# Kernel optimization log

Measured on AMD Instinct MI355X. Metric: run time of the kernel, lower is better.

## Reference

```python
import jax, jax.numpy as jnp
import numpy as np

B, T, D = 32, 4096, 96        # batch, frames, codebook_dim
N_CB, K = 6, 384              # n_codebooks, codebook_size
PROJ, W2V = 192, 768          # semantic_proj_dim, w2v_bert_dim
COMMIT = 0.5


def setup_inputs() -> dict:
    key = jax.random.key(0)
    ks = jax.random.split(key, 7)
    z = jax.random.normal(ks[0], (B, T, D), jnp.float32)
    w2v_targets = jax.random.normal(ks[1], (B, T, W2V), jnp.float32)
    # torch init: uniform(-1/K, 1/K) per codebook
    codebooks = jax.random.uniform(ks[2], (N_CB, K, D), jnp.float32, -1.0 / K, 1.0 / K)
    w1 = jax.random.normal(ks[3], (D, PROJ), jnp.float32) * 0.02
    b1 = jnp.zeros((PROJ,), jnp.float32)
    w2 = jax.random.normal(ks[4], (PROJ, W2V), jnp.float32) * 0.02
    b2 = jnp.zeros((W2V,), jnp.float32)
    return {"z": z, "w2v_targets": w2v_targets, "codebooks": codebooks,
            "w1": w1, "b1": b1, "w2": w2, "b2": b2}


def _quantize(residual, emb):
    """One VQ stage: squared-L2 nearest code + gather. residual: (B,T,D), emb: (K,D)."""
    flat = residual.reshape(-1, D)                                   # (BT, D)
    dist = (jnp.sum(flat * flat, axis=1, keepdims=True)
            - 2.0 * flat @ emb.T
            + jnp.sum(emb * emb, axis=1))                            # (BT, K)
    idx = jnp.argmin(dist, axis=1).reshape(B, T)                     # (B, T)
    z_q = emb[idx]                                                   # (B, T, D) gather
    return z_q, idx


def reference(z, w2v_targets, codebooks, w1, b1, w2, b2):
    sg = jax.lax.stop_gradient
    residual = z
    z_q_total = jnp.zeros_like(z)
    codes = []
    vq_loss = jnp.float32(0.0)
    semantic_loss = jnp.float32(0.0)
    for i in range(N_CB):
        z_q, idx = _quantize(residual, codebooks[i])
        commitment_loss = jnp.mean((sg(z_q) - residual) ** 2)
        embedding_loss = jnp.mean((z_q - sg(residual)) ** 2)
        vq_loss = vq_loss + embedding_loss + COMMIT * commitment_loss
        z_q_st = residual + sg(z_q - residual)                       # straight-through
        if i == 0:
            h = jax.nn.gelu(z_q_st @ w1 + b1, approximate=False)
            pred = h @ w2 + b2                                       # (B, T, W2V)
            semantic_loss = jnp.mean((pred - w2v_targets) ** 2)
        z_q_total = z_q_total + z_q_st
        residual = residual - sg(z_q_st)
        codes.append(idx)
    all_codes = jnp.stack(codes, axis=-1)                            # (B, T, N_CB)
    return z_q_total, all_codes, vq_loss, semantic_loss
```

## Files before the change

kernel.cpp:

```cpp
#include <hip/hip_runtime.h>
#include <hip/hip_bf16.h>

#define BT    131072
#define DD    96
#define KCB   384
#define NCB   6
#define PROJ  192
#define W2V   768

#define ZQT_OFF   0L
#define CODES_OFF 12582912L
#define VQ_OFF    13369344L
#define SEM_OFF   13369345L

#define ACC_OFF   0L
#define E32_OFF   64L
#define W1T_OFF   9280L
#define W2T_OFF   46144L

#define TT 4
#define CT 24
#define TB 256

typedef __attribute__((ext_vector_type(8))) short  bf16x8;
typedef __attribute__((ext_vector_type(4))) float  f32x4;

static __device__ __forceinline__ unsigned short f2bf(float x) {
    __hip_bfloat16 h = __float2bfloat16(x);
    return *reinterpret_cast<unsigned short*>(&h);
}
static __device__ __forceinline__ float comp(const float4& v, int c) {
    return c == 0 ? v.x : c == 1 ? v.y : c == 2 ? v.z : v.w;
}

static __device__ __forceinline__ float pairwise96_sq(const float4* r) {
    float a[8];
#pragma unroll
    for (int j = 0; j < 8; ++j) {
        const int c = j & 3, base = j >> 2;
        float x0 = comp(r[base], c);
        float s  = __fmul_rn(x0, x0);
#pragma unroll
        for (int t = 1; t < 12; ++t) {
            float x = comp(r[base + 2 * t], c);
            s = __fadd_rn(s, __fmul_rn(x, x));
        }
        a[j] = s;
    }
    return __fadd_rn(__fadd_rn(__fadd_rn(a[0], a[1]), __fadd_rn(a[2], a[3])),
                     __fadd_rn(__fadd_rn(a[4], a[5]), __fadd_rn(a[6], a[7])));
}

__global__ void kzero(double* __restrict__ acc) {
    if (threadIdx.x < 8) acc[threadIdx.x] = 0.0;
}

__global__ void kee(const float* __restrict__ cb, float* __restrict__ E32) {
    int c = blockIdx.x * 256 + threadIdx.x;
    if (c < NCB * KCB) {
        const float* row = cb + (size_t)c * DD;
        float a[8];
#pragma unroll
        for (int j = 0; j < 8; ++j) a[j] = __fmul_rn(row[j], row[j]);
        for (int t = 1; t < 12; ++t) {
#pragma unroll
            for (int j = 0; j < 8; ++j) {
                float x = row[8 * t + j];
                a[j] = __fadd_rn(a[j], __fmul_rn(x, x));
            }
        }
        E32[c] = __fadd_rn(__fadd_rn(__fadd_rn(a[0], a[1]), __fadd_rn(a[2], a[3])),
                           __fadd_rn(__fadd_rn(a[4], a[5]), __fadd_rn(a[6], a[7])));
    }
}

__global__ void kwt(const float* __restrict__ w1, const float* __restrict__ w2,
                    __hip_bfloat16* __restrict__ w1T, __hip_bfloat16* __restrict__ w2T) {
    int i = blockIdx.x * 256 + threadIdx.x;
    if (i < DD * PROJ) {
        int n = i / DD, k = i % DD;
        w1T[i] = __float2bfloat16(w1[k * PROJ + n]);
    }
    int j = i - DD * PROJ;
    if (j >= 0 && j < PROJ * W2V) {
        int n = j / PROJ, k = j % PROJ;
        w2T[j] = __float2bfloat16(w2[k * W2V + n]);
    }
}

__global__ __launch_bounds__(256, 2) void kq2(
        const float* __restrict__ z, const float* __restrict__ cb,
        const float* __restrict__ E32, float* __restrict__ dout,
        float4* __restrict__ rg) {
    __shared__ __align__(16) float  e_lds[4][CT * DD];
    __shared__ __align__(16) float2 comb[4][TB];
    __shared__ __align__(16) float  S_lds[TB];

    const int tid = threadIdx.x, lane = tid & 63, w = tid >> 6;
    const long tok0 = (long)blockIdx.x * TB;

    {
        const long t = tok0 + tid;
        const float4* z4 = (const float4*)(z + t * DD);
        float4 r[24];
#pragma unroll
        for (int i = 0; i < 24; ++i) r[i] = z4[i];
        S_lds[tid] = pairwise96_sq(r);
#pragma unroll
        for (int i = 0; i < 24; ++i) rg[(long)i * BT + t] = r[i];
    }
    __syncthreads();

#pragma unroll 1
    for (int s = 0; s < NCB; ++s) {
        float Sj[TT];
#pragma unroll
        for (int j = 0; j < TT; ++j) Sj[j] = S_lds[64 * j + lane];
        float mv[TT]; int bi[TT];
#pragma unroll
        for (int j = 0; j < TT; ++j) { mv[j] = 3.4e38f; bi[j] = 0; }

#pragma unroll 1
        for (int ct = 0; ct < 96 / CT; ++ct) {
            const int cbase = w * 96 + ct * CT;
            {
                const float4* esrc = (const float4*)(cb + ((size_t)s * KCB + cbase) * DD);
                float4* edst = (float4*)&e_lds[w][0];
#pragma unroll
                for (int i = 0; i < 9; ++i) edst[i * 64 + lane] = esrc[i * 64 + lane];
            }
            float acc[CT][TT];
#pragma unroll
            for (int c = 0; c < CT; ++c)
#pragma unroll
                for (int j = 0; j < TT; ++j) acc[c][j] = 0.f;

            float4 rv[TT];
#pragma unroll
            for (int j = 0; j < TT; ++j) rv[j] = rg[tok0 + 64 * j + lane];
#pragma unroll 1
            for (int kt = 0; kt < 24; ++kt) {
                float4 rnx[TT];
                if (kt < 23) {
#pragma unroll
                    for (int j = 0; j < TT; ++j)
                        rnx[j] = rg[(long)(kt + 1) * BT + tok0 + 64 * j + lane];
                }
                float4 r2[TT];
#pragma unroll
                for (int j = 0; j < TT; ++j) {
                    r2[j].x = __fmul_rn(2.f, rv[j].x); r2[j].y = __fmul_rn(2.f, rv[j].y);
                    r2[j].z = __fmul_rn(2.f, rv[j].z); r2[j].w = __fmul_rn(2.f, rv[j].w);
                }
                const float* eb = &e_lds[w][kt * 4];
#pragma unroll
                for (int c = 0; c < CT; ++c) {
                    float4 e = *(const float4*)(eb + c * DD);
#pragma unroll
                    for (int j = 0; j < TT; ++j) {
                        acc[c][j] = fmaf(r2[j].x, e.x, acc[c][j]);
                        acc[c][j] = fmaf(r2[j].y, e.y, acc[c][j]);
                        acc[c][j] = fmaf(r2[j].z, e.z, acc[c][j]);
                        acc[c][j] = fmaf(r2[j].w, e.w, acc[c][j]);
                    }
                }
#pragma unroll
                for (int j = 0; j < TT; ++j) rv[j] = rnx[j];
            }
#pragma unroll
            for (int c = 0; c < CT; ++c) {
                const float E = E32[s * KCB + cbase + c];
#pragma unroll
                for (int j = 0; j < TT; ++j) {
                    float d = __fadd_rn(__fsub_rn(Sj[j], acc[c][j]), E);
                    if (d < mv[j]) { mv[j] = d; bi[j] = cbase + c; }
                }
            }
        }
#pragma unroll
        for (int j = 0; j < TT; ++j)
            comb[w][64 * j + lane] = make_float2(mv[j], (float)bi[j]);
        __syncthreads();

        {
            const long t = tok0 + tid;
            float bv = comb[0][tid].x; int bidx = (int)comb[0][tid].y;
#pragma unroll
            for (int w2 = 1; w2 < 4; ++w2) {
                float2 cnd = comb[w2][tid];
                if (cnd.x < bv) { bv = cnd.x; bidx = (int)cnd.y; }
            }
            dout[CODES_OFF + t * NCB + s] = (float)bidx;
            if (s < NCB - 1) {
                const float4* q4 = (const float4*)(cb + ((size_t)s * KCB + bidx) * DD);
                float4 rn[24];
#pragma unroll
                for (int i = 0; i < 24; ++i) {
                    float4 rv = rg[(long)i * BT + t], q = q4[i];
                    float4 d, st;
                    d.x = __fsub_rn(q.x, rv.x); d.y = __fsub_rn(q.y, rv.y);
                    d.z = __fsub_rn(q.z, rv.z); d.w = __fsub_rn(q.w, rv.w);
                    st.x = __fadd_rn(rv.x, d.x); st.y = __fadd_rn(rv.y, d.y);
                    st.z = __fadd_rn(rv.z, d.z); st.w = __fadd_rn(rv.w, d.w);
                    rn[i].x = __fsub_rn(rv.x, st.x); rn[i].y = __fsub_rn(rv.y, st.y);
                    rn[i].z = __fsub_rn(rv.z, st.z); rn[i].w = __fsub_rn(rv.w, st.w);
                }
                S_lds[tid] = pairwise96_sq(rn);
#pragma unroll
                for (int i = 0; i < 24; ++i) rg[(long)i * BT + t] = rn[i];
            }
        }
        __syncthreads();
    }
}

__global__ __launch_bounds__(256) void kr(
        const float* __restrict__ z, const float* __restrict__ cb,
        const float* __restrict__ codesf, float* __restrict__ zqt_out,
        double* __restrict__ acc) {
    const long tok = (long)blockIdx.x * 256 + threadIdx.x;
    float4 r[24], zqt[24];
    const float4* z4 = (const float4*)(z + tok * DD);
#pragma unroll
    for (int i = 0; i < 24; ++i) r[i] = z4[i];
    double ls[NCB];
#pragma unroll
    for (int s = 0; s < NCB; ++s) {
        const int idx = (int)codesf[tok * NCB + s];
        const float4* q4 = (const float4*)(cb + (size_t)(s * KCB + idx) * DD);
        double a = 0.0;
#pragma unroll
        for (int i = 0; i < 24; ++i) {
            float4 q = q4[i];
            float4 d, st;
            d.x = __fsub_rn(q.x, r[i].x); d.y = __fsub_rn(q.y, r[i].y);
            d.z = __fsub_rn(q.z, r[i].z); d.w = __fsub_rn(q.w, r[i].w);
            st.x = __fadd_rn(r[i].x, d.x); st.y = __fadd_rn(r[i].y, d.y);
            st.z = __fadd_rn(r[i].z, d.z); st.w = __fadd_rn(r[i].w, d.w);
            if (s == 0) {
                zqt[i] = st;
            } else {
                zqt[i].x = __fadd_rn(zqt[i].x, st.x); zqt[i].y = __fadd_rn(zqt[i].y, st.y);
                zqt[i].z = __fadd_rn(zqt[i].z, st.z); zqt[i].w = __fadd_rn(zqt[i].w, st.w);
            }
            r[i].x = __fsub_rn(r[i].x, st.x); r[i].y = __fsub_rn(r[i].y, st.y);
            r[i].z = __fsub_rn(r[i].z, st.z); r[i].w = __fsub_rn(r[i].w, st.w);
            a += (double)d.x * (double)d.x; a += (double)d.y * (double)d.y;
            a += (double)d.z * (double)d.z; a += (double)d.w * (double)d.w;
        }
        ls[s] = a;
    }
    float4* o4 = (float4*)(zqt_out + tok * DD);
#pragma unroll
    for (int i = 0; i < 24; ++i) o4[i] = zqt[i];
#pragma unroll
    for (int s = 0; s < NCB; ++s) {
        double v = ls[s];
        for (int off = 32; off > 0; off >>= 1) v += __shfl_down(v, off, 64);
        if ((threadIdx.x & 63) == 0) atomicAdd(&acc[s], v);
    }
}

__global__ __launch_bounds__(256) void kh(
        const float* __restrict__ z, const float* __restrict__ cb,
        const float* __restrict__ codesf,
        const __hip_bfloat16* __restrict__ w1T, const float* __restrict__ b1,
        const __hip_bfloat16* __restrict__ w2T, const float* __restrict__ b2,
        const float* __restrict__ tgt, double* __restrict__ sem_acc) {
    __shared__ unsigned short hs[64][PROJ + 8];
    const int lane = threadIdx.x & 63, wv = threadIdx.x >> 6;
    const int col  = lane & 15, quad = lane >> 4;
    const long m0  = (long)blockIdx.x * 64 + wv * 16;

    const long tokrow = m0 + col;
    const int  code0  = (int)codesf[tokrow * NCB];
    const float* zr = z  + tokrow * DD;
    const float* qr = cb + (size_t)code0 * DD;
    bf16x8 a1f[3];
#pragma unroll
    for (int ks = 0; ks < 3; ++ks) {
        const int k0 = ks * 32 + quad * 8;
        bf16x8 v;
#pragma unroll
        for (int j = 0; j < 8; ++j) {
            float r = zr[k0 + j], q = qr[k0 + j];
            float d  = __fsub_rn(q, r);
            float st = __fadd_rn(r, d);
            v[j] = (short)f2bf(st);
        }
        a1f[ks] = v;
    }
    for (int nt = 0; nt < 12; ++nt) {
        const int n0 = nt * 16;
        f32x4 accv = {0.f, 0.f, 0.f, 0.f};
        const unsigned short* bw = (const unsigned short*)w1T + (n0 + col) * DD + quad * 8;
#pragma unroll
        for (int ks = 0; ks < 3; ++ks) {
            bf16x8 bf = *(const bf16x8*)(bw + ks * 32);
            accv = __builtin_amdgcn_mfma_f32_16x16x32_bf16(a1f[ks], bf, accv, 0, 0, 0);
        }
#pragma unroll
        for (int r = 0; r < 4; ++r) {
            float x = accv[r] + b1[n0 + col];
            float g = 0.5f * x * (1.0f + erff(x * 0.70710678118654752440f));
            hs[wv * 16 + quad * 4 + r][n0 + col] = f2bf(g);
        }
    }
    __syncthreads();
    bf16x8 a2f[6];
#pragma unroll
    for (int ks = 0; ks < 6; ++ks)
        a2f[ks] = *(const bf16x8*)(&hs[wv * 16 + col][ks * 32 + quad * 8]);
    double lsum = 0.0;
    for (int nt = 0; nt < 48; ++nt) {
        const int n0 = nt * 16;
        f32x4 accv = {0.f, 0.f, 0.f, 0.f};
        const unsigned short* bw = (const unsigned short*)w2T + (size_t)(n0 + col) * PROJ + quad * 8;
#pragma unroll
        for (int ks = 0; ks < 6; ++ks) {
            bf16x8 bf = *(const bf16x8*)(bw + ks * 32);
            accv = __builtin_amdgcn_mfma_f32_16x16x32_bf16(a2f[ks], bf, accv, 0, 0, 0);
        }
#pragma unroll
        for (int r = 0; r < 4; ++r) {
            float pred = accv[r] + b2[n0 + col];
            float dt = pred - tgt[(m0 + quad * 4 + r) * (long)W2V + n0 + col];
            lsum += (double)dt * (double)dt;
        }
    }
    for (int off = 32; off > 0; off >>= 1) lsum += __shfl_down(lsum, off, 64);
    if (lane == 0) atomicAdd(sem_acc, lsum);
}

__global__ void kf(const double* __restrict__ acc, float* __restrict__ dout) {
    if (threadIdx.x == 0 && blockIdx.x == 0) {
        float vq = 0.f;
        for (int s = 0; s < NCB; ++s) {
            float l = (float)(acc[s] / 12582912.0);
            vq = vq + l;
            vq = vq + 0.5f * l;
        }
        dout[VQ_OFF]  = vq;
        dout[SEM_OFF] = (float)(acc[6] / 100663296.0);
    }
}

extern "C" void kernel_launch(void* const* d_in, const int* in_sizes, int n_in,
                              void* d_out, int out_size, void* d_ws, size_t ws_size,
                              hipStream_t stream) {
    const float* z   = (const float*)d_in[0];
    const float* tgt = (const float*)d_in[1];
    const float* cb  = (const float*)d_in[2];
    const float* w1  = (const float*)d_in[3];
    const float* b1  = (const float*)d_in[4];
    const float* w2  = (const float*)d_in[5];
    const float* b2  = (const float*)d_in[6];
    float* out = (float*)d_out;
    char*  ws  = (char*)d_ws;

    double*          accs = (double*)(ws + ACC_OFF);
    float*           E32  = (float*)(ws + E32_OFF);
    __hip_bfloat16*  w1T  = (__hip_bfloat16*)(ws + W1T_OFF);
    __hip_bfloat16*  w2T  = (__hip_bfloat16*)(ws + W2T_OFF);

    kzero<<<dim3(1), dim3(64), 0, stream>>>(accs);
    kee  <<<dim3(9), dim3(256), 0, stream>>>(cb, E32);
    kwt  <<<dim3(648), dim3(256), 0, stream>>>(w1, w2, w1T, w2T);
    kq2  <<<dim3(BT / TB), dim3(256), 0, stream>>>(z, cb, E32, out,
                                                   (float4*)(out + ZQT_OFF));
    kr   <<<dim3(512), dim3(256), 0, stream>>>(z, cb, out + CODES_OFF, out, accs);
    kh   <<<dim3(2048), dim3(256), 0, stream>>>(z, cb, out + CODES_OFF,
                                                w1T, b1, w2T, b2, tgt, accs + 6);
    kf   <<<dim3(1), dim3(64), 0, stream>>>(accs, out);
}
```

Measured before the change: 1.896 ms.

## Split codebook search across 8 waves with smaller code tiles and pre-doubled codes

```diff
diff --git a/kernel.cpp b/kernel.cpp
--- a/kernel.cpp
+++ b/kernel.cpp
@@ -18,8 +18,9 @@
 #define W1T_OFF   9280L
 #define W2T_OFF   46144L
 
+#define WV 8
 #define TT 4
-#define CT 24
+#define CT 16
 #define TB 256
 
 typedef __attribute__((ext_vector_type(8))) short  bf16x8;
@@ -88,18 +89,18 @@
     }
 }
 
-__global__ __launch_bounds__(256, 2) void kq2(
+__global__ __launch_bounds__(512, 4) void kq2(
         const float* __restrict__ z, const float* __restrict__ cb,
         const float* __restrict__ E32, float* __restrict__ dout,
         float4* __restrict__ rg) {
-    __shared__ __align__(16) float  e_lds[4][CT * DD];
-    __shared__ __align__(16) float2 comb[4][TB];
+    __shared__ __align__(16) float  e_lds[WV][CT * DD];
+    __shared__ __align__(16) float2 comb[WV][TB];
     __shared__ __align__(16) float  S_lds[TB];
 
     const int tid = threadIdx.x, lane = tid & 63, w = tid >> 6;
     const long tok0 = (long)blockIdx.x * TB;
 
-    {
+    if (tid < TB) {
         const long t = tok0 + tid;
         const float4* z4 = (const float4*)(z + t * DD);
         float4 r[24];
@@ -121,13 +122,18 @@
         for (int j = 0; j < TT; ++j) { mv[j] = 3.4e38f; bi[j] = 0; }
 
 #pragma unroll 1
-        for (int ct = 0; ct < 96 / CT; ++ct) {
-            const int cbase = w * 96 + ct * CT;
+        for (int ct = 0; ct < 48 / CT; ++ct) {
+            const int cbase = w * 48 + ct * CT;
             {
                 const float4* esrc = (const float4*)(cb + ((size_t)s * KCB + cbase) * DD);
                 float4* edst = (float4*)&e_lds[w][0];
 #pragma unroll
-                for (int i = 0; i < 9; ++i) edst[i * 64 + lane] = esrc[i * 64 + lane];
+                for (int i = 0; i < 6; ++i) {
+                    float4 v = esrc[i * 64 + lane];
+                    v.x = __fmul_rn(2.f, v.x); v.y = __fmul_rn(2.f, v.y);
+                    v.z = __fmul_rn(2.f, v.z); v.w = __fmul_rn(2.f, v.w);
+                    edst[i * 64 + lane] = v;
+                }
             }
             float acc[CT][TT];
 #pragma unroll
@@ -146,22 +152,16 @@
                     for (int j = 0; j < TT; ++j)
                         rnx[j] = rg[(long)(kt + 1) * BT + tok0 + 64 * j + lane];
                 }
-                float4 r2[TT];
-#pragma unroll
-                for (int j = 0; j < TT; ++j) {
-                    r2[j].x = __fmul_rn(2.f, rv[j].x); r2[j].y = __fmul_rn(2.f, rv[j].y);
-                    r2[j].z = __fmul_rn(2.f, rv[j].z); r2[j].w = __fmul_rn(2.f, rv[j].w);
-                }
                 const float* eb = &e_lds[w][kt * 4];
 #pragma unroll
                 for (int c = 0; c < CT; ++c) {
                     float4 e = *(const float4*)(eb + c * DD);
 #pragma unroll
                     for (int j = 0; j < TT; ++j) {
-                        acc[c][j] = fmaf(r2[j].x, e.x, acc[c][j]);
-                        acc[c][j] = fmaf(r2[j].y, e.y, acc[c][j]);
-                        acc[c][j] = fmaf(r2[j].z, e.z, acc[c][j]);
-                        acc[c][j] = fmaf(r2[j].w, e.w, acc[c][j]);
+                        acc[c][j] = fmaf(rv[j].x, e.x, acc[c][j]);
+                        acc[c][j] = fmaf(rv[j].y, e.y, acc[c][j]);
+                        acc[c][j] = fmaf(rv[j].z, e.z, acc[c][j]);
+                        acc[c][j] = fmaf(rv[j].w, e.w, acc[c][j]);
                     }
                 }
 #pragma unroll
@@ -182,11 +182,11 @@
             comb[w][64 * j + lane] = make_float2(mv[j], (float)bi[j]);
         __syncthreads();
 
-        {
+        if (tid < TB) {
             const long t = tok0 + tid;
             float bv = comb[0][tid].x; int bidx = (int)comb[0][tid].y;
 #pragma unroll
-            for (int w2 = 1; w2 < 4; ++w2) {
+            for (int w2 = 1; w2 < WV; ++w2) {
                 float2 cnd = comb[w2][tid];
                 if (cnd.x < bv) { bv = cnd.x; bidx = (int)cnd.y; }
             }
@@ -366,7 +366,7 @@
     kzero<<<dim3(1), dim3(64), 0, stream>>>(accs);
     kee  <<<dim3(9), dim3(256), 0, stream>>>(cb, E32);
     kwt  <<<dim3(648), dim3(256), 0, stream>>>(w1, w2, w1T, w2T);
-    kq2  <<<dim3(BT / TB), dim3(256), 0, stream>>>(z, cb, E32, out,
+    kq2  <<<dim3(BT / TB), dim3(512), 0, stream>>>(z, cb, E32, out,
                                                    (float4*)(out + ZQT_OFF));
     kr   <<<dim3(512), dim3(256), 0, stream>>>(z, cb, out + CODES_OFF, out, accs);
     kh   <<<dim3(2048), dim3(256), 0, stream>>>(z, cb, out + CODES_OFF,
```

Result: slower. 1.955 ms (+3.1%).
